# Optimization experiments

Measured on AMD Instinct MI355X. Metric: run time of the kernel, lower is better.

## Reference

```python
import jax, jax.numpy as jnp
import numpy as np

BS, N, IN_F, OUT_F, HEADS = 32, 512, 256, 128, 4
NEG_SLOPE = 0.2


def setup_inputs() -> dict:
    key = jax.random.key(0)
    k1, k2, k3, k4, k5 = jax.random.split(key, 5)
    inputs = jax.random.normal(k1, (BS, N, IN_F), dtype=jnp.float32)
    adj = (jax.random.uniform(k2, (BS, N, N)) > 0.5).astype(jnp.float32)
    # xavier_normal-style init with relu gain sqrt(2)
    w = jax.random.normal(k3, (IN_F, HEADS * OUT_F), dtype=jnp.float32) * (
        np.sqrt(2.0) * np.sqrt(2.0 / (IN_F + HEADS * OUT_F))
    )
    a_i = jax.random.normal(k4, (HEADS, OUT_F, 1), dtype=jnp.float32) * (
        np.sqrt(2.0) * np.sqrt(2.0 / (OUT_F + 1))
    )
    a_j = jax.random.normal(k5, (HEADS, OUT_F, 1), dtype=jnp.float32) * (
        np.sqrt(2.0) * np.sqrt(2.0 / (OUT_F + 1))
    )
    bias = jnp.zeros((HEADS * OUT_F,), dtype=jnp.float32)
    return {"inputs": inputs, "adj": adj, "w": w, "a_i": a_i, "a_j": a_j, "bias": bias}


def reference(inputs, adj, w, a_i, a_j, bias):
    bs, n, _ = inputs.shape
    H, D = a_i.shape[0], a_i.shape[1]
    # self_loop_type == 2: adjacency unchanged
    # project: [bs, n, H, D]
    h = jnp.matmul(inputs, w).reshape(bs, n, H, D)
    # additive attention coefficients: [bs, n, H]
    coeff_i = jnp.einsum('bnhd,hdo->bnho', h, a_i)[..., 0]
    coeff_j = jnp.einsum('bnhd,hdo->bnho', h, a_j)[..., 0]
    # broadcast-sum scores e[b, i, j, h], leaky relu
    e = jax.nn.leaky_relu(coeff_i[:, :, None, :] + coeff_j[:, None, :, :],
                          negative_slope=NEG_SLOPE)
    adj_h = adj[..., None]  # [bs, n, n, 1], broadcasts over heads
    masked_e = jnp.where(adj_h <= 0, jnp.float32(-1e9), e)
    # softmax over neighbor axis j (dim 2), then re-mask
    attention = jax.nn.softmax(masked_e, axis=2) * adj_h
    # dropout = 0.0 -> no-op; normalize=False, average=False
    # per-head aggregation, all heads at once: out[b,i,h,d] = sum_j att[b,i,j,h] h[b,j,h,d]
    out = jnp.einsum('bijh,bjhd->bihd', attention, h).reshape(bs, n, H * D)
    return out + bias
```

## Files before the change

### kernel.cpp

```cpp
#include <hip/hip_runtime.h>

#define BSZ 32
#define NN 512
#define INF 256
#define NH 4
#define HD 512
#define NEG_SLOPE 0.2f

typedef __attribute__((ext_vector_type(8))) short bf16x8;
typedef __attribute__((ext_vector_type(8))) unsigned short ushort8;
typedef __attribute__((ext_vector_type(4))) float f32x4;

static __device__ __forceinline__ unsigned short f2bf(float f) {
    unsigned u = __builtin_bit_cast(unsigned, f);
    return (unsigned short)((u + 0x7FFFu + ((u >> 16) & 1u)) >> 16);
}

static __device__ __forceinline__ bf16x8 pk8(float4 a, float4 b) {
    unsigned d0, d1, d2, d3;
    asm("v_cvt_pk_bf16_f32 %0, %1, %2" : "=v"(d0) : "v"(a.x), "v"(a.y));
    asm("v_cvt_pk_bf16_f32 %0, %1, %2" : "=v"(d1) : "v"(a.z), "v"(a.w));
    asm("v_cvt_pk_bf16_f32 %0, %1, %2" : "=v"(d2) : "v"(b.x), "v"(b.y));
    asm("v_cvt_pk_bf16_f32 %0, %1, %2" : "=v"(d3) : "v"(b.z), "v"(b.w));
    uint4 u; u.x = d0; u.y = d1; u.z = d2; u.w = d3;
    return __builtin_bit_cast(bf16x8, u);
}

static __device__ __forceinline__ void gl_lds16(const void* g, void* l) {
    __builtin_amdgcn_global_load_lds(
        (const __attribute__((address_space(1))) unsigned int*)g,
        (__attribute__((address_space(3))) unsigned int*)l, 16, 0, 0);
}

__global__ __launch_bounds__(256) void k_prep(
    const float* __restrict__ w, unsigned short* __restrict__ wB,
    const float* __restrict__ adj, unsigned char* __restrict__ mbB)
{
    const int bid = blockIdx.x;
    if (bid < 2048) {
        const int lane = threadIdx.x & 63, wave = threadIdx.x >> 6;
        const int row0 = bid * 8 + wave * 2;
        #pragma unroll
        for (int rr = 0; rr < 2; ++rr) {
            const float* ap = adj + (size_t)(row0 + rr) * NN + lane * 8;
            float4 a0 = *(const float4*)ap;
            float4 a1 = *(const float4*)(ap + 4);
            unsigned byte = 0;
            byte |= (a0.x > 0.f) ? 1u : 0u;  byte |= (a0.y > 0.f) ? 2u : 0u;
            byte |= (a0.z > 0.f) ? 4u : 0u;  byte |= (a0.w > 0.f) ? 8u : 0u;
            byte |= (a1.x > 0.f) ? 16u : 0u; byte |= (a1.y > 0.f) ? 32u : 0u;
            byte |= (a1.z > 0.f) ? 64u : 0u; byte |= (a1.w > 0.f) ? 128u : 0u;
            mbB[(size_t)(row0 + rr) * 64 + lane] = (unsigned char)byte;
        }
    } else {
        int gid = (bid - 2048) * 256 + threadIdx.x;
        int c = gid & 511, k = gid >> 9;
        int kb = k >> 5, g = (k >> 3) & 3, e = k & 7;
        wB[(((size_t)(kb * 4 + g) * 512) + c) * 8 + e] = f2bf(w[(size_t)k * 512 + c]);
    }
}

__global__ __launch_bounds__(256) void k_proj(
    const float* __restrict__ x, const unsigned short* __restrict__ wB,
    const float* __restrict__ ai, const float* __restrict__ aj,
    unsigned short* __restrict__ hB, float* __restrict__ ciT, float* __restrict__ cjT)
{
    __shared__ unsigned short hs[NH * 4096];
    const int tid = threadIdx.x;
    const int lane = tid & 63, head = tid >> 6;
    const int l15 = lane & 15, g = lane >> 4;
    const int row0 = blockIdx.x * 32;

    f32x4 acc[2][8] = {};
    const float* xp0 = x + (size_t)(row0 + l15) * INF + g * 8;
    const float* xp1 = xp0 + 16 * INF;
    const unsigned short* bp = wB + ((size_t)g * 512 + head * 128 + l15) * 8;

    #pragma unroll
    for (int kb = 0; kb < 8; ++kb) {
        float4 f0 = *(const float4*)(xp0 + kb * 32);
        float4 f1 = *(const float4*)(xp0 + kb * 32 + 4);
        float4 f2 = *(const float4*)(xp1 + kb * 32);
        float4 f3 = *(const float4*)(xp1 + kb * 32 + 4);
        bf16x8 a0 = pk8(f0, f1);
        bf16x8 a1 = pk8(f2, f3);
        #pragma unroll
        for (int nf = 0; nf < 8; ++nf) {
            bf16x8 bv = *(const bf16x8*)(bp + (size_t)kb * 16384 + nf * 128);
            acc[0][nf] = __builtin_amdgcn_mfma_f32_16x16x32_bf16(a0, bv, acc[0][nf], 0, 0, 0);
            acc[1][nf] = __builtin_amdgcn_mfma_f32_16x16x32_bf16(a1, bv, acc[1][nf], 0, 0, 0);
        }
    }

    float aiv[8], ajv[8];
    #pragma unroll
    for (int nf = 0; nf < 8; ++nf) {
        aiv[nf] = ai[head * 128 + nf * 16 + l15];
        ajv[nf] = aj[head * 128 + nf * 16 + l15];
    }
    const int b = row0 >> 9;
    const int nloc0 = row0 & 511;
    const int kb2 = nloc0 >> 5;

    #pragma unroll
    for (int m = 0; m < 2; ++m) {
        float pi[4] = {0,0,0,0}, pj[4] = {0,0,0,0};
        #pragma unroll
        for (int nf = 0; nf < 8; ++nf)
            #pragma unroll
            for (int reg = 0; reg < 4; ++reg) {
                pi[reg] = fmaf(acc[m][nf][reg], aiv[nf], pi[reg]);
                pj[reg] = fmaf(acc[m][nf][reg], ajv[nf], pj[reg]);
            }
        #pragma unroll
        for (int reg = 0; reg < 4; ++reg) {
            #pragma unroll
            for (int off = 1; off < 16; off <<= 1) {
                pi[reg] += __shfl_xor(pi[reg], off);
                pj[reg] += __shfl_xor(pj[reg], off);
            }
        }
        if (l15 == 0) {
            #pragma unroll
            for (int reg = 0; reg < 4; ++reg) {
                int n = nloc0 + 16 * m + 4 * g + reg;
                ciT[((size_t)(head * BSZ + b) * NN) + n] = pi[reg];
                cjT[((size_t)(head * BSZ + b) * NN) + n] = pj[reg];
            }
        }
        #pragma unroll
        for (int reg = 0; reg < 4; ++reg) {
            int jloc = 16 * m + 4 * g + reg;
            int g2 = jloc >> 3, e = jloc & 7;
            #pragma unroll
            for (int nf = 0; nf < 8; ++nf)
                hs[head * 4096 + nf * 512 + g2 * 128 + l15 * 8 + e] =
                    f2bf(acc[m][nf][reg]);
        }
    }
    __syncthreads();
    {
        ushort8* dst = (ushort8*)(hB + (((size_t)(b * 4 + head) * 16 + kb2) * 4096));
        const ushort8* src = (const ushort8*)(hs + head * 4096);
        #pragma unroll
        for (int it = 0; it < 8; ++it)
            dst[it * 64 + lane] = src[it * 64 + lane];
    }
}

__global__ __launch_bounds__(256, 4) void k_attn(
    const unsigned short* __restrict__ hB, const float* __restrict__ ciT,
    const float* __restrict__ cjT, const unsigned* __restrict__ mb,
    const float* __restrict__ bias, float* __restrict__ out)
{
    __shared__ __align__(16) unsigned short Bst[4][4096];
    __shared__ __align__(16) float cjh[NN];
    __shared__ float cih[64];
    __shared__ unsigned maskS[64][17];
    __shared__ float Mpart[4];

    const int tid = threadIdx.x;
    const int lane = tid & 63, wave = tid >> 6;
    const int l15 = lane & 15, g = lane >> 4;

    const int orig = blockIdx.x;
    const int swz = (orig & 7) * 128 + (orig >> 3);
    const int b  = swz >> 5;
    const int h  = (swz >> 3) & 3;
    const int i0 = (swz & 7) * 64;

    const char* gslab = (const char*)(hB + (size_t)(b * NH + h) * 65536);

    #pragma unroll
    for (int s = 0; s < 3; ++s) {
        const char* gs = gslab + (size_t)s * 8192 + wave * 2048 + lane * 16;
        char* ld = (char*)&Bst[s][0] + wave * 2048;
        gl_lds16(gs, ld);
        gl_lds16(gs + 1024, ld + 1024);
    }

    {
        const float* src = cjT + (size_t)(h * BSZ + b) * NN;
        float v0 = src[tid], v1 = src[tid + 256];
        cjh[tid] = v0; cjh[tid + 256] = v1;
        float mv = fmaxf(v0, v1);
        #pragma unroll
        for (int off = 32; off; off >>= 1) mv = fmaxf(mv, __shfl_xor(mv, off));
        if (lane == 0) Mpart[wave] = mv;
        if (tid < 64) cih[tid] = ciT[(size_t)(h * BSZ + b) * NN + i0 + tid];
        uint4 m4 = ((const uint4*)(mb + ((size_t)b * NN + i0) * 16))[tid];
        int base = tid * 4, row = base >> 4, wi = base & 15;
        maskS[row][wi] = m4.x; maskS[row][wi + 1] = m4.y;
        maskS[row][wi + 2] = m4.z; maskS[row][wi + 3] = m4.w;
    }
    __syncthreads();

    const float M = fmaxf(fmaxf(Mpart[0], Mpart[1]), fmaxf(Mpart[2], Mpart[3]));
    const float bc = cih[wave * 16 + l15];
    float smx = bc + M;
    const float mrow = fmaxf(smx, NEG_SLOPE * smx);

    float bvv[8];
    #pragma unroll
    for (int nf = 0; nf < 8; ++nf) bvv[nf] = bias[h * 128 + nf * 16 + l15];

    bf16x8 ones;
    #pragma unroll
    for (int e = 0; e < 8; ++e) ones[e] = (short)0x3F80;

    f32x4 acc[8] = {};
    f32x4 accs = {};
    const unsigned* mrowp = maskS[wave * 16 + l15];

    #pragma unroll
    for (int kb = 0; kb < 16; ++kb) {
        const int rem = 15 - kb;
        if (rem >= 2)      asm volatile("s_waitcnt vmcnt(4)" ::: "memory");
        else if (rem == 1) asm volatile("s_waitcnt vmcnt(2)" ::: "memory");
        else               asm volatile("s_waitcnt vmcnt(0)" ::: "memory");
        __builtin_amdgcn_s_barrier();
        __builtin_amdgcn_sched_barrier(0);

        if (kb + 3 < 16) {
            const char* gs = gslab + (size_t)(kb + 3) * 8192 + wave * 2048 + lane * 16;
            char* ld = (char*)&Bst[(kb + 3) & 3][0] + wave * 2048;
            gl_lds16(gs, ld);
            gl_lds16(gs + 1024, ld + 1024);
        }

        float4 cva = *(const float4*)&cjh[kb * 32 + g * 8];
        float4 cvb = *(const float4*)&cjh[kb * 32 + g * 8 + 4];
        float cj8[8] = {cva.x, cva.y, cva.z, cva.w, cvb.x, cvb.y, cvb.z, cvb.w};
        unsigned byte = (mrowp[kb] >> (g * 8)) & 0xFFu;
        float p[8];
        #pragma unroll
        for (int e = 0; e < 8; ++e) {
            float s = bc + cj8[e];
            s = fmaxf(s, NEG_SLOPE * s);
            float pe = __expf(s - mrow);
            p[e] = ((byte >> e) & 1u) ? pe : 0.f;
        }
        unsigned d0, d1, d2, d3;
        asm("v_cvt_pk_bf16_f32 %0, %1, %2" : "=v"(d0) : "v"(p[0]), "v"(p[1]));
        asm("v_cvt_pk_bf16_f32 %0, %1, %2" : "=v"(d1) : "v"(p[2]), "v"(p[3]));
        asm("v_cvt_pk_bf16_f32 %0, %1, %2" : "=v"(d2) : "v"(p[4]), "v"(p[5]));
        asm("v_cvt_pk_bf16_f32 %0, %1, %2" : "=v"(d3) : "v"(p[6]), "v"(p[7]));
        uint4 u; u.x = d0; u.y = d1; u.z = d2; u.w = d3;
        bf16x8 av = __builtin_bit_cast(bf16x8, u);

        const char* bb = (const char*)&Bst[kb & 3][0] + lane * 16;
        bf16x8 bfr[8];
        #pragma unroll
        for (int nf = 0; nf < 8; ++nf)
            bfr[nf] = *(const bf16x8*)(bb + nf * 1024);

        #pragma unroll
        for (int nf = 0; nf < 8; ++nf)
            acc[nf] = __builtin_amdgcn_mfma_f32_16x16x32_bf16(av, bfr[nf], acc[nf], 0, 0, 0);
        accs = __builtin_amdgcn_mfma_f32_16x16x32_bf16(av, ones, accs, 0, 0, 0);
    }

    #pragma unroll
    for (int reg = 0; reg < 4; ++reg) {
        float sum = accs[reg];
        float inv = sum > 0.f ? 1.f / sum : 0.f;
        const int i = i0 + wave * 16 + g * 4 + reg;
        #pragma unroll
        for (int nf = 0; nf < 8; ++nf) {
            int colg = h * 128 + nf * 16 + l15;
            out[(size_t)(b * NN + i) * HD + colg] = acc[nf][reg] * inv + bvv[nf];
        }
    }
}

extern "C" void kernel_launch(void* const* d_in, const int* in_sizes, int n_in,
                              void* d_out, int out_size, void* d_ws, size_t ws_size,
                              hipStream_t stream)
{
    const float* x    = (const float*)d_in[0];
    const float* adj  = (const float*)d_in[1];
    const float* w    = (const float*)d_in[2];
    const float* ai   = (const float*)d_in[3];
    const float* aj   = (const float*)d_in[4];
    const float* bias = (const float*)d_in[5];
    float* out = (float*)d_out;

    char* ws = (char*)d_ws;
    unsigned short* wB = (unsigned short*)ws;
    unsigned short* hB = (unsigned short*)(ws + 262144);
    float* ciT         = (float*)(ws + 17039360);
    float* cjT         = (float*)(ws + 17301504);
    unsigned char* mbB = (unsigned char*)(ws + 17563648);

    k_prep<<<2560, 256, 0, stream>>>(w, wB, adj, mbB);
    k_proj<<<BSZ * NN / 32, 256, 0, stream>>>(x, wB, ai, aj, hB, ciT, cjT);
    k_attn<<<BSZ * NH * (NN / 64), 256, 0, stream>>>(hB, ciT, cjT,
                                                     (const unsigned*)mbB, bias, out);
}
```

Baseline: 49.67 us.

## Switch attention B-tile staging to double-buffered 4-slab chunks with fewer barriers

Replaces the 4-deep ring of single 8KB slabs, which needed a barrier on every k-step, with two 32KB buffers that each hold four slabs. The next chunk is prefetched while the current one is consumed, and blocks synchronise once per four k-steps. This doubles LDS per block and lowers launch bounds to 2 blocks per CU. The aim is to cut barrier and wait overhead, but it costs occupancy and fine-grained load/compute overlap. It also depends on __syncthreads to wait for the asynchronous global-to-LDS copies.

```diff
diff --git a/kernel.cpp b/kernel.cpp
--- a/kernel.cpp
+++ b/kernel.cpp
@@ -148,12 +148,12 @@
     }
 }
 
-__global__ __launch_bounds__(256, 4) void k_attn(
+__global__ __launch_bounds__(256, 2) void k_attn(
     const unsigned short* __restrict__ hB, const float* __restrict__ ciT,
     const float* __restrict__ cjT, const unsigned* __restrict__ mb,
     const float* __restrict__ bias, float* __restrict__ out)
 {
-    __shared__ __align__(16) unsigned short Bst[4][4096];
+    __shared__ __align__(16) unsigned short Bst[2][16384];
     __shared__ __align__(16) float cjh[NN];
     __shared__ float cih[64];
     __shared__ unsigned maskS[64][17];
@@ -172,9 +172,9 @@
     const char* gslab = (const char*)(hB + (size_t)(b * NH + h) * 65536);
 
     #pragma unroll
-    for (int s = 0; s < 3; ++s) {
-        const char* gs = gslab + (size_t)s * 8192 + wave * 2048 + lane * 16;
-        char* ld = (char*)&Bst[s][0] + wave * 2048;
+    for (int sl = 0; sl < 4; ++sl) {
+        const char* gs = gslab + (size_t)sl * 8192 + wave * 2048 + lane * 16;
+        char* ld = (char*)&Bst[0][0] + sl * 8192 + wave * 2048;
         gl_lds16(gs, ld);
         gl_lds16(gs + 1024, ld + 1024);
     }
@@ -210,54 +210,55 @@
 
     f32x4 acc[8] = {};
     f32x4 accs = {};
+    int cur = 0;
     const unsigned* mrowp = maskS[wave * 16 + l15];
 
     #pragma unroll
-    for (int kb = 0; kb < 16; ++kb) {
-        const int rem = 15 - kb;
-        if (rem >= 2)      asm volatile("s_waitcnt vmcnt(4)" ::: "memory");
-        else if (rem == 1) asm volatile("s_waitcnt vmcnt(2)" ::: "memory");
-        else               asm volatile("s_waitcnt vmcnt(0)" ::: "memory");
-        __builtin_amdgcn_s_barrier();
-        __builtin_amdgcn_sched_barrier(0);
-
-        if (kb + 3 < 16) {
-            const char* gs = gslab + (size_t)(kb + 3) * 8192 + wave * 2048 + lane * 16;
-            char* ld = (char*)&Bst[(kb + 3) & 3][0] + wave * 2048;
-            gl_lds16(gs, ld);
-            gl_lds16(gs + 1024, ld + 1024);
-        }
-
-        float4 cva = *(const float4*)&cjh[kb * 32 + g * 8];
-        float4 cvb = *(const float4*)&cjh[kb * 32 + g * 8 + 4];
-        float cj8[8] = {cva.x, cva.y, cva.z, cva.w, cvb.x, cvb.y, cvb.z, cvb.w};
-        unsigned byte = (mrowp[kb] >> (g * 8)) & 0xFFu;
-        float p[8];
-        #pragma unroll
-        for (int e = 0; e < 8; ++e) {
-            float s = bc + cj8[e];
-            s = fmaxf(s, NEG_SLOPE * s);
-            float pe = __expf(s - mrow);
-            p[e] = ((byte >> e) & 1u) ? pe : 0.f;
-        }
-        unsigned d0, d1, d2, d3;
-        asm("v_cvt_pk_bf16_f32 %0, %1, %2" : "=v"(d0) : "v"(p[0]), "v"(p[1]));
-        asm("v_cvt_pk_bf16_f32 %0, %1, %2" : "=v"(d1) : "v"(p[2]), "v"(p[3]));
-        asm("v_cvt_pk_bf16_f32 %0, %1, %2" : "=v"(d2) : "v"(p[4]), "v"(p[5]));
-        asm("v_cvt_pk_bf16_f32 %0, %1, %2" : "=v"(d3) : "v"(p[6]), "v"(p[7]));
-        uint4 u; u.x = d0; u.y = d1; u.z = d2; u.w = d3;
-        bf16x8 av = __builtin_bit_cast(bf16x8, u);
-
-        const char* bb = (const char*)&Bst[kb & 3][0] + lane * 16;
-        bf16x8 bfr[8];
-        #pragma unroll
-        for (int nf = 0; nf < 8; ++nf)
-            bfr[nf] = *(const bf16x8*)(bb + nf * 1024);
-
-        #pragma unroll
-        for (int nf = 0; nf < 8; ++nf)
-            acc[nf] = __builtin_amdgcn_mfma_f32_16x16x32_bf16(av, bfr[nf], acc[nf], 0, 0, 0);
-        accs = __builtin_amdgcn_mfma_f32_16x16x32_bf16(av, ones, accs, 0, 0, 0);
+    for (int p = 0; p < 4; ++p) {
+        if (p < 3) {
+            #pragma unroll
+            for (int sl = 0; sl < 4; ++sl) {
+                const char* gs = gslab + (size_t)(p * 4 + 4 + sl) * 8192
+                                 + wave * 2048 + lane * 16;
+                char* ld = (char*)&Bst[cur ^ 1][0] + sl * 8192 + wave * 2048;
+                gl_lds16(gs, ld);
+                gl_lds16(gs + 1024, ld + 1024);
+            }
+        }
+
+        #pragma unroll
+        for (int kk = 0; kk < 4; ++kk) {
+            const int kb = p * 4 + kk;
+            float4 cva = *(const float4*)&cjh[kb * 32 + g * 8];
+            float4 cvb = *(const float4*)&cjh[kb * 32 + g * 8 + 4];
+            float cj8[8] = {cva.x, cva.y, cva.z, cva.w, cvb.x, cvb.y, cvb.z, cvb.w};
+            unsigned byte = (mrowp[kb] >> (g * 8)) & 0xFFu;
+            float pr[8];
+            #pragma unroll
+            for (int e = 0; e < 8; ++e) {
+                float s = bc + cj8[e];
+                s = fmaxf(s, NEG_SLOPE * s);
+                float pe = __expf(s - mrow);
+                pr[e] = ((byte >> e) & 1u) ? pe : 0.f;
+            }
+            unsigned d0, d1, d2, d3;
+            asm("v_cvt_pk_bf16_f32 %0, %1, %2" : "=v"(d0) : "v"(pr[0]), "v"(pr[1]));
+            asm("v_cvt_pk_bf16_f32 %0, %1, %2" : "=v"(d1) : "v"(pr[2]), "v"(pr[3]));
+            asm("v_cvt_pk_bf16_f32 %0, %1, %2" : "=v"(d2) : "v"(pr[4]), "v"(pr[5]));
+            asm("v_cvt_pk_bf16_f32 %0, %1, %2" : "=v"(d3) : "v"(pr[6]), "v"(pr[7]));
+            uint4 u; u.x = d0; u.y = d1; u.z = d2; u.w = d3;
+            bf16x8 av = __builtin_bit_cast(bf16x8, u);
+
+            const char* bb = (const char*)&Bst[cur][0] + kk * 8192 + lane * 16;
+            #pragma unroll
+            for (int nf = 0; nf < 8; ++nf) {
+                bf16x8 bv = *(const bf16x8*)(bb + nf * 1024);
+                acc[nf] = __builtin_amdgcn_mfma_f32_16x16x32_bf16(av, bv, acc[nf], 0, 0, 0);
+            }
+            accs = __builtin_amdgcn_mfma_f32_16x16x32_bf16(av, ones, accs, 0, 0, 0);
+        }
+
+        if (p < 3) { __syncthreads(); cur ^= 1; }
     }
 
     #pragma unroll
```

New measurement: 55.81 us. 12.3% more time.
